# Optimization experiments

Hardware: AMD Instinct MI355X
Metric: run time of the kernel (lower is better)

The kernel has to match this reference:

```python
import jax, jax.numpy as jnp
import numpy as np

EPS = 1e-5  # torch LayerNorm default

def _ln(x, g, b):
    mu = jnp.mean(x, -1, keepdims=True)
    var = jnp.mean((x - mu) ** 2, -1, keepdims=True)
    return (x - mu) * jax.lax.rsqrt(var + EPS) * g + b

def _xavier(key, shape):
    fan_in, fan_out = shape[-2], shape[-1]
    s = (2.0 / (fan_in + fan_out)) ** 0.5
    return jax.random.normal(key, shape, dtype=jnp.float32) * s

def setup_inputs() -> dict:
    key = jax.random.key(0)
    ks = jax.random.split(key, 24)
    N, E, B = 10000, 160000, 64
    D, M, FF, K = 128, 32, 32, 5
    EIN = 2 * FF + 1 + 2 * D          # 321
    inp = {}
    inp["coords"] = jax.random.normal(ks[0], (N, 3), dtype=jnp.float32)
    inp["atomids"] = jax.random.randint(ks[1], (N,), 0, 11)
    inp["edge_index"] = jax.random.randint(ks[2], (2, E), 0, N)
    inp["batch"] = jnp.sort(jax.random.randint(ks[3], (N,), 0, B))
    inp["num_graphs"] = B
    inp["emb"] = _xavier(ks[4], (11, D))
    # stacked per-kernel EGNN params (leading dim K=5)
    inp["keW1"] = _xavier(ks[5], (K, EIN, 2 * EIN)); inp["keb1"] = jnp.zeros((K, 2 * EIN))
    inp["keW2"] = _xavier(ks[6], (K, 2 * EIN, M));   inp["keb2"] = jnp.zeros((K, M))
    inp["keng"] = jnp.ones((K, M));   inp["kenb"] = jnp.zeros((K, M))
    inp["kn1g"] = jnp.ones((K, D));   inp["kn1b"] = jnp.zeros((K, D))
    inp["knW1"] = _xavier(ks[7], (K, D + M, 2 * D)); inp["knb1"] = jnp.zeros((K, 2 * D))
    inp["knW2"] = _xavier(ks[8], (K, 2 * D, D));     inp["knb2"] = jnp.zeros((K, D))
    inp["kn2g"] = jnp.ones((K, D));   inp["kn2b"] = jnp.zeros((K, D))
    # fnn: (K+1)*D = 768 -> 256 -> 256 -> 256
    inp["fW0"] = _xavier(ks[9], ((K + 1) * D, 256)); inp["fb0"] = jnp.zeros((256,))
    inp["fW1"] = _xavier(ks[10], (256, 256));        inp["fb1"] = jnp.zeros((256,))
    inp["fW2"] = _xavier(ks[11], (256, 256));        inp["fb2"] = jnp.zeros((256,))
    # fnn2: 256 -> 256 -> 256 -> 1
    inp["gW0"] = _xavier(ks[12], (256, 256));        inp["gb0"] = jnp.zeros((256,))
    inp["gW1"] = _xavier(ks[13], (256, 256));        inp["gb1"] = jnp.zeros((256,))
    inp["gW2"] = _xavier(ks[14], (256, 1));          inp["gb2"] = jnp.zeros((1,))
    return inp

def reference(coords, atomids, edge_index, batch, num_graphs, emb,
              keW1, keb1, keW2, keb2, keng, kenb, kn1g, kn1b,
              knW1, knb1, knW2, knb2, kn2g, kn2b,
              fW0, fb0, fW1, fb1, fW2, fb2,
              gW0, gb0, gW1, gb1, gW2, gb2):
    silu = jax.nn.silu
    N = coords.shape[0]
    src, dst = edge_index[0], edge_index[1]  # x_j = x[src], x_i = x[dst]
    feats = emb[atomids]                                  # [N,128]
    # coords are never updated across kernels -> fourier edge attr computed once
    rel = coords[src] - coords[dst]                       # [E,3]
    d = jnp.sum(rel * rel, -1, keepdims=True)             # [E,1] squared distance
    scales = 2.0 ** jnp.arange(32, dtype=coords.dtype)
    xs = d / scales                                       # [E,32]
    ea = jnp.concatenate([jnp.sin(xs), jnp.cos(xs), d], -1)  # [E,65]
    ones_e = jnp.ones((src.shape[0], 1), feats.dtype)
    deg = jax.ops.segment_sum(ones_e, dst, num_segments=N)   # [N,1]
    deg = jnp.maximum(deg, 1.0)
    feat_list = [feats]
    for k in range(keW1.shape[0]):
        # edge message MLP
        m = jnp.concatenate([feats[dst], feats[src], ea], -1)        # [E,321]
        h = silu(m @ keW1[k] + keb1[k])                              # [E,642]
        m_ij = silu(h @ keW2[k] + keb2[k])                           # [E,32]
        m_ij = _ln(m_ij, keng[k], kenb[k])
        # scatter-mean aggregate to target nodes
        m_i = jax.ops.segment_sum(m_ij, dst, num_segments=N) / deg   # [N,32]
        m_i = _ln(m_i, keng[k], kenb[k])  # (original reuses edge_norm1)
        # node update MLP with residual
        hf = _ln(feats, kn1g[k], kn1b[k])
        h2 = silu(jnp.concatenate([hf, m_i], -1) @ knW1[k] + knb1[k])
        h2 = h2 @ knW2[k] + knb2[k]
        h2 = _ln(h2, kn2g[k], kn2b[k])
        feats = feats + h2
        feat_list.append(feats)
    f = silu(jnp.concatenate(feat_list, -1))              # [N,768]
    f = silu(f @ fW0 + fb0)
    f = silu(f @ fW1 + fb1)
    f = silu(f @ fW2 + fb2)
    gs = jax.ops.segment_sum(f, batch, num_segments=num_graphs)
    gc = jax.ops.segment_sum(jnp.ones((N, 1), f.dtype), batch, num_segments=num_graphs)
    g = gs / jnp.maximum(gc, 1.0)                         # [B,256] scatter_mean
    g = silu(g @ gW0 + gb0)
    g = silu(g @ gW1 + gb1)
    return g @ gW2 + gb2                                  # [B,1]
```

## Files before the change

kernel.cpp:

```cpp
#include <hip/hip_runtime.h>
#include <cstdint>
#include <cstddef>


#define DEV __device__ __forceinline__

typedef __attribute__((ext_vector_type(8))) short bf16x8;
typedef __attribute__((ext_vector_type(4))) float f32x4;

DEV float siluf(float x) { return x / (1.f + __expf(-x)); }

DEV unsigned short f2bf(float f) {
  unsigned u = __float_as_uint(f);
  unsigned r = u + 0x7FFFu + ((u >> 16) & 1u);
  return (unsigned short)(r >> 16);
}
DEV float bf2f(unsigned short h) { return __uint_as_float(((unsigned)h) << 16); }

DEV f32x4 mfma16(bf16x8 a, bf16x8 b, f32x4 c) {
  return __builtin_amdgcn_mfma_f32_16x16x32_bf16(a, b, c, 0, 0, 0);
}

DEV void unpack8(bf16x8 v, float* o) {
#pragma unroll
  for (int j = 0; j < 8; ++j) o[j] = bf2f((unsigned short)v[j]);
}

__global__ __launch_bounds__(256) void k_gather(const int* __restrict__ atomids,
                                                const float* __restrict__ emb,
                                                float* __restrict__ feats_all,
                                                unsigned short* __restrict__ fH, int N) {
  int idx = blockIdx.x * 256 + threadIdx.x;
  if (idx >= N * 128) return;
  int i = idx >> 7, j = idx & 127;
  float v = emb[atomids[i] * 128 + j];
  size_t o = (size_t)i * 768 + j;
  feats_all[o] = v;
  fH[o] = f2bf(v);
}

__global__ __launch_bounds__(256) void k_edge_prep(const float* __restrict__ coords,
                                                   const int* __restrict__ ei, int E,
                                                   float* __restrict__ d_arr,
                                                   int* __restrict__ cnt) {
  int e = blockIdx.x * 256 + threadIdx.x;
  if (e >= E) return;
  int s = ei[e], t = ei[E + e];
  float dx = coords[3 * s + 0] - coords[3 * t + 0];
  float dy = coords[3 * s + 1] - coords[3 * t + 1];
  float dz = coords[3 * s + 2] - coords[3 * t + 2];
  d_arr[e] = dx * dx + dy * dy + dz * dz;
  atomicAdd(&cnt[t], 1);
}

__global__ __launch_bounds__(1024) void k_scan2(const int* __restrict__ cnt, int N,
                                                int* __restrict__ cursor,
                                                float* __restrict__ degf) {
  __shared__ int wsum[16];
  int tid = threadIdx.x;
  int chunk = (N + 1023) >> 10;
  int lo = tid * chunk, hi = min(N, lo + chunk);
  int s = 0;
  for (int i = lo; i < hi; ++i) s += cnt[i];
  int lane = tid & 63, wv = tid >> 6;
  int v = s;
#pragma unroll
  for (int off = 1; off < 64; off <<= 1) {
    int u = __shfl_up(v, off, 64);
    if (lane >= off) v += u;
  }
  if (lane == 63) wsum[wv] = v;
  __syncthreads();
  if (wv == 0 && lane < 16) {
    int w = wsum[lane];
#pragma unroll
    for (int off = 1; off < 16; off <<= 1) {
      int u = __shfl_up(w, off, 16);
      if (lane >= off) w += u;
    }
    wsum[lane] = w;
  }
  __syncthreads();
  int run = (wv ? wsum[wv - 1] : 0) + v - s;
  for (int i = lo; i < hi; ++i) {
    int c = cnt[i];
    cursor[i] = run;
    degf[i] = fmaxf((float)c, 1.f);
    run += c;
  }
}

__global__ __launch_bounds__(256) void k_scatter(const int* __restrict__ ei, int E,
                                                 const float* __restrict__ d_arr,
                                                 int* __restrict__ cursor,
                                                 int* __restrict__ ssrc,
                                                 int* __restrict__ sdst,
                                                 float* __restrict__ sd) {
  int e = blockIdx.x * 256 + threadIdx.x;
  if (e >= E) return;
  int s = ei[e], t = ei[E + e];
  int p = atomicAdd(&cursor[t], 1);
  ssrc[p] = s;
  sdst[p] = t;
  sd[p] = d_arr[e];
}

struct PPJob {
  const float* W;
  unsigned short* hi;
  unsigned short* lo;
  unsigned long long wStride, oStride;
  int ldw, K, Kpad, Nc, Npad, layers;
};
struct PPJobs { PPJob j[11]; };

__global__ __launch_bounds__(256) void k_prepack_all(PPJobs jobs) {
  PPJob jb = jobs.j[blockIdx.y];
  long long per = (long long)jb.Npad * jb.Kpad;
  long long idx = (long long)blockIdx.x * 256 + threadIdx.x;
  if (idx >= per * jb.layers) return;
  int layer = (int)(idx / per);
  int r = (int)(idx - (long long)layer * per);
  const float* W = jb.W + (size_t)layer * jb.wStride;
  int n = r / jb.Kpad, k = r - n * jb.Kpad;
  float v = (n < jb.Nc && k < jb.K) ? W[(size_t)k * jb.ldw + n] : 0.f;
  unsigned short h = f2bf(v);
  jb.hi[(size_t)layer * jb.oStride + r] = h;
  jb.lo[(size_t)layer * jb.oStride + r] = f2bf(v - bf2f(h));
}

__global__ __launch_bounds__(256) void gemm_bf(
    const unsigned short* __restrict__ AH, int lda,
    const unsigned short* __restrict__ BH, const unsigned short* __restrict__ BL, int ldb,
    const float* __restrict__ bias,
    float* __restrict__ C, int ldc,
    unsigned short* __restrict__ CH, int ldch,
    int M, int Ncols, int K, int actOut, int actA) {
  const int t = threadIdx.x;
  const int wave = t >> 6, lane = t & 63;
  const int nl = lane & 15, quad = lane >> 4;
  const int bm = blockIdx.x * 64 + wave * 16;
  const int bn = blockIdx.y * 64;
  f32x4 zero = {0.f, 0.f, 0.f, 0.f};
  f32x4 acc[4] = {zero, zero, zero, zero};
  for (int kb = 0; kb < K; kb += 32) {
    bf16x8 ah;
    int row = bm + nl;
    if (row < M) {
      ah = *(const bf16x8*)(AH + (size_t)row * lda + kb + quad * 8);
      if (actA) {
#pragma unroll
        for (int j = 0; j < 8; ++j)
          ah[j] = (short)f2bf(siluf(bf2f((unsigned short)ah[j])));
      }
    } else {
#pragma unroll
      for (int j = 0; j < 8; ++j) ah[j] = 0;
    }
#pragma unroll
    for (int tn = 0; tn < 4; ++tn) {
      size_t boff = (size_t)(bn + tn * 16 + nl) * ldb + kb + quad * 8;
      bf16x8 bh = *(const bf16x8*)(BH + boff);
      bf16x8 bl = *(const bf16x8*)(BL + boff);
      acc[tn] = mfma16(ah, bh, acc[tn]);
      acc[tn] = mfma16(ah, bl, acc[tn]);
    }
  }
#pragma unroll
  for (int tn = 0; tn < 4; ++tn) {
    int c = bn + tn * 16 + nl;
    float bv = (bias && c < Ncols) ? bias[c] : 0.f;
#pragma unroll
    for (int r = 0; r < 4; ++r) {
      int rr = bm + quad * 4 + r;
      if (rr >= M) continue;
      float v = acc[tn][r] + bv;
      if (actOut) v = siluf(v);
      if (C && c < Ncols) C[(size_t)rr * ldc + c] = v;
      if (CH && c < Ncols) CH[(size_t)rr * ldch + c] = f2bf(v);
    }
  }
}

__global__ __launch_bounds__(256) void gemm_proj(
    const unsigned short* __restrict__ AH, int lda,
    const unsigned short* __restrict__ B1H, const unsigned short* __restrict__ B1L,
    const unsigned short* __restrict__ B2H, const unsigned short* __restrict__ B2L,
    const float* __restrict__ bias1,
    unsigned short* __restrict__ C1, unsigned short* __restrict__ C2,
    int planeN, int M) {
  const int y = blockIdx.y;
  const unsigned short* BH;
  const unsigned short* BL;
  const float* bias;
  unsigned short* CP;
  int yp;
  if (y < 11) { BH = B1H; BL = B1L; bias = bias1; CP = C1; yp = y; }
  else        { BH = B2H; BL = B2L; bias = nullptr; CP = C2; yp = y - 11; }
  const int t = threadIdx.x;
  const int wave = t >> 6, lane = t & 63;
  const int nl = lane & 15, quad = lane >> 4;
  const int bm = blockIdx.x * 128 + wave * 32;
  const int bn = yp * 64;
  f32x4 zero = {0.f, 0.f, 0.f, 0.f};
  f32x4 acc[2][4] = {{zero, zero, zero, zero}, {zero, zero, zero, zero}};
  for (int kb = 0; kb < 128; kb += 32) {
    bf16x8 ah[2];
#pragma unroll
    for (int h = 0; h < 2; ++h) {
      int row = bm + h * 16 + nl;
      if (row < M)
        ah[h] = *(const bf16x8*)(AH + (size_t)row * lda + kb + quad * 8);
      else
#pragma unroll
        for (int j = 0; j < 8; ++j) ah[h][j] = 0;
    }
#pragma unroll
    for (int tn = 0; tn < 4; ++tn) {
      size_t boff = (size_t)(bn + tn * 16 + nl) * 128 + kb + quad * 8;
      bf16x8 bh = *(const bf16x8*)(BH + boff);
      bf16x8 bl = *(const bf16x8*)(BL + boff);
#pragma unroll
      for (int h = 0; h < 2; ++h) {
        acc[h][tn] = mfma16(ah[h], bh, acc[h][tn]);
        acc[h][tn] = mfma16(ah[h], bl, acc[h][tn]);
      }
    }
  }
#pragma unroll
  for (int h = 0; h < 2; ++h) {
#pragma unroll
    for (int tn = 0; tn < 4; ++tn) {
      int c = bn + tn * 16 + nl;
      float bv = (bias && c < 642) ? bias[c] : 0.f;
#pragma unroll
      for (int r = 0; r < 4; ++r) {
        int rr = bm + h * 16 + quad * 4 + r;
        if (rr >= M) continue;
        CP[(size_t)yp * planeN + (size_t)rr * 64 + tn * 16 + nl] =
            f2bf(acc[h][tn][r] + bv);
      }
    }
  }
}

__global__ __launch_bounds__(256, 3) void k_edge_mfma(
    const unsigned short* __restrict__ Ap, const unsigned short* __restrict__ Bp,
    int planeN,
    const int* __restrict__ ssrc, const int* __restrict__ sdst,
    const float* __restrict__ sd_g, int E,
    const unsigned short* __restrict__ WeaT,
    const float* __restrict__ Wea64,
    const unsigned short* __restrict__ W2T,
    const float* __restrict__ b2v,
    const float* __restrict__ eng, const float* __restrict__ enb,
    float* __restrict__ msum) {
  __shared__ float sAB[4][16 * 68];
  __shared__ unsigned short sHh[4][16 * 72];
  __shared__ float sDs[64];
  __shared__ int sSrcS[64], sDstS[64];

  const int t = threadIdx.x;
  const int wave = t >> 6, lane = t & 63;
  const int nl = lane & 15, quad = lane >> 4;
  const int e0 = blockIdx.x * 64;

  if (lane < 16) {
    int el = wave * 16 + lane;
    int e = e0 + el;
    int ec = (e < E) ? e : (E - 1);
    sSrcS[el] = ssrc[ec];
    sDstS[el] = sdst[ec];
    sDs[el] = sd_g[ec];
  }
  const int r = lane >> 2, cq = lane & 3;
  const int elr = wave * 16 + r;
  const size_t aOff = (size_t)sDstS[elr] * 64 + cq * 16;
  const size_t bOff = (size_t)sSrcS[elr] * 64 + cq * 16;
  const float dR = sDs[elr];
  float* myAB = sAB[wave];
  unsigned short* myH = sHh[wave];

  bf16x8 pa0, pa1, pb0, pb1;
  bf16x8 w1[4][2], w2a[2][2], w2b[2][2];

  auto loadW1 = [&](int c) {
#pragma unroll
    for (int tn = 0; tn < 4; ++tn)
#pragma unroll
      for (int ks = 0; ks < 2; ++ks)
        w1[tn][ks] = *(const bf16x8*)(WeaT + (size_t)(c * 64 + tn * 16 + nl) * 64 +
                                      ks * 32 + quad * 8);
  };
  auto loadW2 = [&](int c, bf16x8(*w)[2]) {
#pragma unroll
    for (int tn = 0; tn < 2; ++tn)
#pragma unroll
      for (int ks = 0; ks < 2; ++ks)
        w[tn][ks] = *(const bf16x8*)(W2T + (size_t)(tn * 16 + nl) * 704 + c * 64 +
                                     ks * 32 + quad * 8);
  };
  auto issue = [&](int c) {
    const unsigned short* a = Ap + (size_t)c * planeN + aOff;
    const unsigned short* b = Bp + (size_t)c * planeN + bOff;
    pa0 = *(const bf16x8*)a;
    pa1 = *(const bf16x8*)(a + 8);
    pb0 = *(const bf16x8*)b;
    pb1 = *(const bf16x8*)(b + 8);
  };
  auto commit = [&](int c) {
    float za[16], zb[16], w[16];
    unpack8(pa0, za); unpack8(pa1, za + 8);
    unpack8(pb0, zb); unpack8(pb1, zb + 8);
    const int cb = c * 64 + cq * 16;
    if (cb + 15 < 642) {
#pragma unroll
      for (int j = 0; j < 4; ++j) {
        f32x4 wv = *(const f32x4*)(Wea64 + cb + 4 * j);
        w[4 * j] = wv.x; w[4 * j + 1] = wv.y; w[4 * j + 2] = wv.z; w[4 * j + 3] = wv.w;
      }
    } else {
#pragma unroll
      for (int u = 0; u < 16; ++u) w[u] = (cb + u < 642) ? Wea64[cb + u] : 0.f;
    }
#pragma unroll
    for (int j = 0; j < 4; ++j) {
      f32x4 o;
#pragma unroll
      for (int u = 0; u < 4; ++u) o[u] = za[4 * j + u] + zb[4 * j + u] + dR * w[4 * j + u];
      *(f32x4*)(myAB + r * 68 + cq * 16 + 4 * j) = o;
    }
  };

  issue(0);
  bf16x8 eaHi[2];
  {
    float d = sDs[wave * 16 + nl];
#pragma unroll
    for (int ks = 0; ks < 2; ++ks)
#pragma unroll
      for (int j = 0; j < 8; ++j) {
        int k = ks * 32 + quad * 8 + j;
        float arg = d * exp2f(-(float)(k & 31));
        float v = (k < 32) ? __sinf(arg) : __cosf(arg);
        eaHi[ks][j] = (short)f2bf(v);
      }
  }
  loadW1(0);
  loadW2(0, w2a);

  f32x4 zero = {0.f, 0.f, 0.f, 0.f};
  f32x4 macc[2] = {zero, zero};

#pragma unroll
  for (int c = 0; c < 11; ++c) {
    commit(c);
    if (c < 10) issue(c + 1);
    f32x4 acc1[4] = {zero, zero, zero, zero};
#pragma unroll
    for (int tn = 0; tn < 4; ++tn)
#pragma unroll
      for (int ks = 0; ks < 2; ++ks) acc1[tn] = mfma16(eaHi[ks], w1[tn][ks], acc1[tn]);
#pragma unroll
    for (int tn = 0; tn < 4; ++tn)
#pragma unroll
      for (int rr = 0; rr < 4; ++rr) {
        int lrow = quad * 4 + rr;
        float z = acc1[tn][rr] + myAB[lrow * 68 + tn * 16 + nl];
        myH[lrow * 72 + tn * 16 + nl] = f2bf(siluf(z));
      }
    if (c < 10) {
      loadW1(c + 1);
      loadW2(c + 1, (c & 1) ? w2a : w2b);
    }
    bf16x8(*w2)[2] = (c & 1) ? w2b : w2a;
#pragma unroll
    for (int ks = 0; ks < 2; ++ks) {
      bf16x8 ah = *(const bf16x8*)(myH + nl * 72 + ks * 32 + quad * 8);
#pragma unroll
      for (int tn = 0; tn < 2; ++tn) macc[tn] = mfma16(ah, w2[tn][ks], macc[tn]);
    }
  }

  float g0 = eng[nl], g1v = eng[16 + nl], bb0 = enb[nl], bb1 = enb[16 + nl];
  float bi0 = b2v[nl], bi1 = b2v[16 + nl];
  float* sMw = myAB;
#pragma unroll
  for (int rr = 0; rr < 4; ++rr) {
    float v0 = siluf(macc[0][rr] + bi0);
    float v1 = siluf(macc[1][rr] + bi1);
    float s = v0 + v1;
    float ss = v0 * v0 + v1 * v1;
#pragma unroll
    for (int m = 1; m < 16; m <<= 1) {
      s += __shfl_xor(s, m, 16);
      ss += __shfl_xor(ss, m, 16);
    }
    float mu = s * (1.f / 32.f);
    float var = ss * (1.f / 32.f) - mu * mu;
    float rs = rsqrtf(var + 1e-5f);
    int lr = quad * 4 + rr;
    sMw[lr * 33 + nl] = (v0 - mu) * rs * g0 + bb0;
    sMw[lr * 33 + 16 + nl] = (v1 - mu) * rs * g1v + bb1;
  }
  __syncthreads();
  {
    int col = t & 31, seg = t >> 5;
    float acc = 0.f;
    int cur = -1;
#pragma unroll
    for (int i = 0; i < 8; ++i) {
      int e = seg * 8 + i;
      int dn = (e0 + e < E) ? sDstS[e] : -1;
      if (dn != cur) {
        if (cur >= 0) atomicAdd(&msum[(size_t)cur * 32 + col], acc);
        acc = 0.f;
        cur = dn;
      }
      if (dn >= 0) acc += sAB[e >> 4][(e & 15) * 33 + col];
    }
    if (cur >= 0) atomicAdd(&msum[(size_t)cur * 32 + col], acc);
  }
}

__global__ __launch_bounds__(256) void k_node_ln(
    const float* __restrict__ msum, const float* __restrict__ deg,
    const float* __restrict__ featsAll, int k,
    const float* __restrict__ n1g, const float* __restrict__ n1b,
    const float* __restrict__ eng, const float* __restrict__ enb,
    unsigned short* __restrict__ hcatH, int N) {
  int node = blockIdx.x * 4 + (threadIdx.x >> 6);
  int lane = threadIdx.x & 63;
  if (node >= N) return;
  const float* fr = featsAll + (size_t)node * 768 + k * 128;
  float x0 = fr[lane], x1 = fr[64 + lane];
  float s = x0 + x1;
#pragma unroll
  for (int m = 1; m < 64; m <<= 1) s += __shfl_xor(s, m, 64);
  float mu = s * (1.f / 128.f);
  float d0 = x0 - mu, d1 = x1 - mu;
  float v = d0 * d0 + d1 * d1;
#pragma unroll
  for (int m = 1; m < 64; m <<= 1) v += __shfl_xor(v, m, 64);
  float rstd = rsqrtf(v * (1.f / 128.f) + 1e-5f);
  size_t hb = (size_t)node * 160;
  hcatH[hb + lane] = f2bf(d0 * rstd * n1g[lane] + n1b[lane]);
  hcatH[hb + 64 + lane] = f2bf(d1 * rstd * n1g[64 + lane] + n1b[64 + lane]);
  float dg = deg[node];
  int col = lane & 31;
  float y = msum[(size_t)node * 32 + col] / dg;
  float sy = y;
#pragma unroll
  for (int m = 1; m < 32; m <<= 1) sy += __shfl_xor(sy, m, 32);
  float mu2 = sy * (1.f / 32.f);
  float dy = y - mu2;
  float vy = dy * dy;
#pragma unroll
  for (int m = 1; m < 32; m <<= 1) vy += __shfl_xor(vy, m, 32);
  float rstd2 = rsqrtf(vy * (1.f / 32.f) + 1e-5f);
  if (lane < 32) hcatH[hb + 128 + col] = f2bf(dy * rstd2 * eng[col] + enb[col]);
}

__global__ __launch_bounds__(256) void k_n2_resid(
    const unsigned short* __restrict__ t1H,
    const unsigned short* __restrict__ BH, const unsigned short* __restrict__ BL,
    const float* __restrict__ b2,
    const float* __restrict__ n2g, const float* __restrict__ n2b,
    float* __restrict__ featsAll, unsigned short* __restrict__ fH, int k, int N) {
  const int t = threadIdx.x;
  const int wave = t >> 6, lane = t & 63;
  const int nl = lane & 15, quad = lane >> 4;
  const int bm = blockIdx.x * 64 + wave * 16;
  f32x4 zero = {0.f, 0.f, 0.f, 0.f};
  f32x4 acc[8] = {zero, zero, zero, zero, zero, zero, zero, zero};
  for (int kb = 0; kb < 256; kb += 32) {
    bf16x8 ah;
    int row = bm + nl;
    if (row < N)
      ah = *(const bf16x8*)(t1H + (size_t)row * 256 + kb + quad * 8);
    else
#pragma unroll
      for (int j = 0; j < 8; ++j) ah[j] = 0;
#pragma unroll
    for (int tn = 0; tn < 8; ++tn) {
      size_t boff = (size_t)(tn * 16 + nl) * 256 + kb + quad * 8;
      bf16x8 bh = *(const bf16x8*)(BH + boff);
      bf16x8 bl = *(const bf16x8*)(BL + boff);
      acc[tn] = mfma16(ah, bh, acc[tn]);
      acc[tn] = mfma16(ah, bl, acc[tn]);
    }
  }
  float bv[8], gv[8], bb[8];
#pragma unroll
  for (int tn = 0; tn < 8; ++tn) {
    int col = tn * 16 + nl;
    bv[tn] = b2[col];
    gv[tn] = n2g[col];
    bb[tn] = n2b[col];
  }
#pragma unroll
  for (int r = 0; r < 4; ++r) {
    int row = bm + quad * 4 + r;
    float v[8];
    float s = 0.f, ss = 0.f;
#pragma unroll
    for (int tn = 0; tn < 8; ++tn) {
      v[tn] = acc[tn][r] + bv[tn];
      s += v[tn];
      ss += v[tn] * v[tn];
    }
#pragma unroll
    for (int m = 1; m < 16; m <<= 1) {
      s += __shfl_xor(s, m, 16);
      ss += __shfl_xor(ss, m, 16);
    }
    float mu = s * (1.f / 128.f);
    float var = ss * (1.f / 128.f) - mu * mu;
    float rs = rsqrtf(var + 1e-5f);
    if (row < N) {
      const float* fk = featsAll + (size_t)row * 768 + k * 128;
      size_t ob = (size_t)row * 768 + (k + 1) * 128;
#pragma unroll
      for (int tn = 0; tn < 8; ++tn) {
        int col = tn * 16 + nl;
        float o = fk[col] + (v[tn] - mu) * rs * gv[tn] + bb[tn];
        featsAll[ob + col] = o;
        fH[ob + col] = f2bf(o);
      }
    }
  }
}

__global__ __launch_bounds__(256) void k_pool2(const float* __restrict__ f,
                                               const int* __restrict__ batch,
                                               float* __restrict__ gsum,
                                               float* __restrict__ gcnt, int N) {
  int n0 = blockIdx.x * 64;
  int col = threadIdx.x;
  float acc = 0.f;
  int cur = -1;
  for (int i = 0; i < 64; ++i) {
    int n = n0 + i;
    if (n >= N) break;
    int b = batch[n];
    if (b != cur) {
      if (cur >= 0) atomicAdd(&gsum[cur * 256 + col], acc);
      acc = 0.f;
      cur = b;
    }
    acc += f[(size_t)n * 256 + col];
  }
  if (cur >= 0) atomicAdd(&gsum[cur * 256 + col], acc);
  if (threadIdx.x == 0) {
    int cnt = 0;
    cur = -1;
    for (int i = 0; i < 64; ++i) {
      int n = n0 + i;
      if (n >= N) break;
      int b = batch[n];
      if (b != cur) {
        if (cur >= 0) atomicAdd(&gcnt[cur], (float)cnt);
        cnt = 0;
        cur = b;
      }
      cnt++;
    }
    if (cur >= 0) atomicAdd(&gcnt[cur], (float)cnt);
  }
}

__global__ void k_gdiv(float* gsum, const float* gcnt, unsigned short* gH) {
  int b = blockIdx.x, j = threadIdx.x;
  float v = gsum[b * 256 + j] / fmaxf(gcnt[b], 1.f);
  gH[b * 256 + j] = f2bf(v);
}

__global__ void k_gout(const float* __restrict__ g2, const float* __restrict__ gW2,
                       const float* __restrict__ gb2, float* __restrict__ out) {
  int b = threadIdx.x;
  if (b >= 64) return;
  float s = gb2[0];
  for (int j = 0; j < 256; ++j) s += g2[b * 256 + j] * gW2[j];
  out[b] = s;
}

extern "C" void kernel_launch(void* const* d_in, const int* in_sizes, int n_in,
                              void* d_out, int out_size, void* d_ws, size_t ws_size,
                              hipStream_t stream) {
  const float* coords = (const float*)d_in[0];
  const int* atomids = (const int*)d_in[1];
  const int* ei = (const int*)d_in[2];
  const int* batch = (const int*)d_in[3];
  const float* emb = (const float*)d_in[5];
  const float* keW1 = (const float*)d_in[6];
  const float* keb1 = (const float*)d_in[7];
  const float* keW2 = (const float*)d_in[8];
  const float* keb2 = (const float*)d_in[9];
  const float* keng = (const float*)d_in[10];
  const float* kenb = (const float*)d_in[11];
  const float* kn1g = (const float*)d_in[12];
  const float* kn1b = (const float*)d_in[13];
  const float* knW1 = (const float*)d_in[14];
  const float* knb1 = (const float*)d_in[15];
  const float* knW2 = (const float*)d_in[16];
  const float* knb2 = (const float*)d_in[17];
  const float* kn2g = (const float*)d_in[18];
  const float* kn2b = (const float*)d_in[19];
  const float* fW0 = (const float*)d_in[20];
  const float* fb0 = (const float*)d_in[21];
  const float* fW1 = (const float*)d_in[22];
  const float* fb1 = (const float*)d_in[23];
  const float* fW2 = (const float*)d_in[24];
  const float* fb2 = (const float*)d_in[25];
  const float* gW0 = (const float*)d_in[26];
  const float* gb0 = (const float*)d_in[27];
  const float* gW1 = (const float*)d_in[28];
  const float* gb1 = (const float*)d_in[29];
  const float* gW2 = (const float*)d_in[30];
  const float* gb2 = (const float*)d_in[31];

  const int N = in_sizes[0] / 3;
  const int E = in_sizes[2] / 2;
  const int planeN = N * 64;

  size_t off = 0;
  auto alloc = [&](size_t n) {
    float* p = (float*)d_ws + off;
    off += (n + 63) & ~(size_t)63;
    return p;
  };
  float* feats_all = alloc((size_t)N * 768);
  float* d_arr = alloc(E);
  float* degf = alloc(N);
  float* msum = alloc((size_t)N * 32);
  float* f1 = alloc((size_t)N * 256);
  float* gsum = alloc(64 * 256);
  float* gcnt = alloc(64);
  float* g2 = alloc(64 * 256);
  int* cnt = (int*)alloc(N);
  int* cursor = (int*)alloc(N);
  int* ssrc = (int*)alloc(E);
  int* sdst = (int*)alloc(E);
  float* sd = alloc(E);

  unsigned short* ubase = (unsigned short*)(alloc(0));
  size_t uoff = 0;
  auto ualloc = [&](size_t n) {
    unsigned short* p = ubase + uoff;
    uoff += (n + 63) & ~(size_t)63;
    return p;
  };
  unsigned short* fH = ualloc((size_t)N * 768);
  unsigned short* ApU = ualloc((size_t)11 * planeN);
  unsigned short* BpU = ualloc((size_t)11 * planeN);
  unsigned short* hcatH = ualloc((size_t)N * 160);
  unsigned short* t1H = ualloc((size_t)N * 256);
  unsigned short* fAH = ualloc((size_t)N * 256);
  unsigned short* fBH = ualloc((size_t)N * 256);
  unsigned short* gH = ualloc(64 * 256);
  unsigned short* g1H = ualloc(64 * 256);
  const size_t sDst_ = 704 * 128, sSrc_ = 704 * 128, sEa_ = 704 * 64;
  const size_t sW2_ = 32 * 704, sN1_ = 256 * 160, sN2_ = 128 * 256;
  unsigned short* PdstH = ualloc(5 * sDst_); unsigned short* PdstL = ualloc(5 * sDst_);
  unsigned short* PsrcH = ualloc(5 * sSrc_); unsigned short* PsrcL = ualloc(5 * sSrc_);
  unsigned short* PeaH = ualloc(5 * sEa_);   unsigned short* PeaL = ualloc(5 * sEa_);
  unsigned short* PW2H = ualloc(5 * sW2_);   unsigned short* PW2L = ualloc(5 * sW2_);
  unsigned short* Pn1H = ualloc(5 * sN1_);   unsigned short* Pn1L = ualloc(5 * sN1_);
  unsigned short* Pn2H = ualloc(5 * sN2_);   unsigned short* Pn2L = ualloc(5 * sN2_);
  unsigned short* Pf0H = ualloc(256 * 768);  unsigned short* Pf0L = ualloc(256 * 768);
  unsigned short* Pf1H = ualloc(256 * 256);  unsigned short* Pf1L = ualloc(256 * 256);
  unsigned short* Pf2H = ualloc(256 * 256);  unsigned short* Pf2L = ualloc(256 * 256);
  unsigned short* Pg0H = ualloc(256 * 256);  unsigned short* Pg0L = ualloc(256 * 256);
  unsigned short* Pg1H = ualloc(256 * 256);  unsigned short* Pg1L = ualloc(256 * 256);

  PPJobs jobs;
  auto setJob = [&](int i, const float* W, size_t wStr, int ldw, int K, int Kpad,
                    int Nc, int Npad, unsigned short* hi, unsigned short* lo,
                    size_t oStr, int layers) {
    jobs.j[i] = PPJob{W, hi, lo, (unsigned long long)wStr, (unsigned long long)oStr,
                      ldw, K, Kpad, Nc, Npad, layers};
  };
  setJob(0, keW1, (size_t)321 * 642, 642, 128, 128, 642, 704, PdstH, PdstL, sDst_, 5);
  setJob(1, keW1 + 128 * 642, (size_t)321 * 642, 642, 128, 128, 642, 704, PsrcH, PsrcL, sSrc_, 5);
  setJob(2, keW1 + 256 * 642, (size_t)321 * 642, 642, 64, 64, 642, 704, PeaH, PeaL, sEa_, 5);
  setJob(3, keW2, (size_t)642 * 32, 32, 642, 704, 32, 32, PW2H, PW2L, sW2_, 5);
  setJob(4, knW1, (size_t)160 * 256, 256, 160, 160, 256, 256, Pn1H, Pn1L, sN1_, 5);
  setJob(5, knW2, (size_t)256 * 128, 128, 256, 256, 128, 128, Pn2H, Pn2L, sN2_, 5);
  setJob(6, fW0, 0, 256, 768, 768, 256, 256, Pf0H, Pf0L, 0, 1);
  setJob(7, fW1, 0, 256, 256, 256, 256, 256, Pf1H, Pf1L, 0, 1);
  setJob(8, fW2, 0, 256, 256, 256, 256, 256, Pf2H, Pf2L, 0, 1);
  setJob(9, gW0, 0, 256, 256, 256, 256, 256, Pg0H, Pg0L, 0, 1);
  setJob(10, gW1, 0, 256, 256, 256, 256, 256, Pg1H, Pg1L, 0, 1);
  k_prepack_all<<<dim3(1760, 11), 256, 0, stream>>>(jobs);

  k_gather<<<(N * 128 + 255) / 256, 256, 0, stream>>>(atomids, emb, feats_all, fH, N);
  hipMemsetAsync(cnt, 0, (size_t)N * sizeof(int), stream);
  k_edge_prep<<<(E + 255) / 256, 256, 0, stream>>>(coords, ei, E, d_arr, cnt);
  k_scan2<<<1, 1024, 0, stream>>>(cnt, N, cursor, degf);
  k_scatter<<<(E + 255) / 256, 256, 0, stream>>>(ei, E, d_arr, cursor, ssrc, sdst, sd);

  const int MT128 = (N + 127) / 128;
  const int MT64 = (N + 63) / 64;
  for (int k = 0; k < 5; ++k) {
    gemm_proj<<<dim3(MT128, 22), 256, 0, stream>>>(
        fH + k * 128, 768,
        PdstH + k * sDst_, PdstL + k * sDst_,
        PsrcH + k * sSrc_, PsrcL + k * sSrc_,
        keb1 + k * 642, ApU, BpU, planeN, N);
    hipMemsetAsync(msum, 0, (size_t)N * 32 * sizeof(float), stream);
    k_edge_mfma<<<(E + 63) / 64, 256, 0, stream>>>(
        ApU, BpU, planeN, ssrc, sdst, sd, E,
        PeaH + k * sEa_,
        keW1 + (size_t)k * 321 * 642 + (size_t)320 * 642,
        PW2H + k * sW2_,
        keb2 + k * 32, keng + k * 32, kenb + k * 32, msum);
    k_node_ln<<<(N + 3) / 4, 256, 0, stream>>>(
        msum, degf, feats_all, k, kn1g + k * 128, kn1b + k * 128,
        keng + k * 32, kenb + k * 32, hcatH, N);
    gemm_bf<<<dim3(MT64, 4), 256, 0, stream>>>(
        hcatH, 160, Pn1H + k * sN1_, Pn1L + k * sN1_, 160,
        knb1 + k * 256, nullptr, 0, t1H, 256, N, 256, 160, 1, 0);
    k_n2_resid<<<MT64, 256, 0, stream>>>(
        t1H, Pn2H + k * sN2_, Pn2L + k * sN2_, knb2 + k * 128,
        kn2g + k * 128, kn2b + k * 128, feats_all, fH, k, N);
  }

  gemm_bf<<<dim3(MT64, 4), 256, 0, stream>>>(
      fH, 768, Pf0H, Pf0L, 768, fb0, nullptr, 0, fAH, 256, N, 256, 768, 1, 1);
  gemm_bf<<<dim3(MT64, 4), 256, 0, stream>>>(
      fAH, 256, Pf1H, Pf1L, 256, fb1, nullptr, 0, fBH, 256, N, 256, 256, 1, 0);
  gemm_bf<<<dim3(MT64, 4), 256, 0, stream>>>(
      fBH, 256, Pf2H, Pf2L, 256, fb2, f1, 256, nullptr, 0, N, 256, 256, 1, 0);

  hipMemsetAsync(gsum, 0, 64 * 256 * sizeof(float), stream);
  hipMemsetAsync(gcnt, 0, 64 * sizeof(float), stream);
  k_pool2<<<(N + 63) / 64, 256, 0, stream>>>(f1, batch, gsum, gcnt, N);
  k_gdiv<<<64, 256, 0, stream>>>(gsum, gcnt, gH);
  gemm_bf<<<dim3(1, 4), 256, 0, stream>>>(
      gH, 256, Pg0H, Pg0L, 256, gb0, nullptr, 0, g1H, 256, 64, 256, 256, 1, 0);
  gemm_bf<<<dim3(1, 4), 256, 0, stream>>>(
      g1H, 256, Pg1H, Pg1L, 256, gb1, g2, 256, nullptr, 0, 64, 256, 256, 1, 0);
  k_gout<<<1, 64, 0, stream>>>(g2, gW2, gb2, (float*)d_out);
}
```

Measured before the change: 1.808 ms.

## Deepen edge-kernel prefetch to two stages and fuse dst/src projection tiles

The edge MFMA kernel now double-buffers both the gathered A/B projection rows and the W2 fragments, issuing loads two chunks ahead instead of one, so gather latency is hidden behind more compute. gemm_proj is restructured so each block handles 64 rows and computes both the dst and src projections for the same column slice, sharing one A-fragment load across eight accumulator tiles instead of splitting the work across separate grid-y blocks. The msum memset is moved before the projection GEMM. The cost is higher register pressure in both kernels, which may reduce occupancy.

```diff
diff --git a/kernel.cpp b/kernel.cpp
--- a/kernel.cpp
+++ b/kernel.cpp
@@ -189,57 +189,43 @@
     const float* __restrict__ bias1,
     unsigned short* __restrict__ C1, unsigned short* __restrict__ C2,
     int planeN, int M) {
-  const int y = blockIdx.y;
-  const unsigned short* BH;
-  const unsigned short* BL;
-  const float* bias;
-  unsigned short* CP;
-  int yp;
-  if (y < 11) { BH = B1H; BL = B1L; bias = bias1; CP = C1; yp = y; }
-  else        { BH = B2H; BL = B2L; bias = nullptr; CP = C2; yp = y - 11; }
+  const int yp = blockIdx.y;
   const int t = threadIdx.x;
   const int wave = t >> 6, lane = t & 63;
   const int nl = lane & 15, quad = lane >> 4;
-  const int bm = blockIdx.x * 128 + wave * 32;
-  const int bn = yp * 64;
+  const int bm = blockIdx.x * 64 + wave * 16;
   f32x4 zero = {0.f, 0.f, 0.f, 0.f};
-  f32x4 acc[2][4] = {{zero, zero, zero, zero}, {zero, zero, zero, zero}};
+  f32x4 acc[8] = {zero, zero, zero, zero, zero, zero, zero, zero};
   for (int kb = 0; kb < 128; kb += 32) {
-    bf16x8 ah[2];
-#pragma unroll
-    for (int h = 0; h < 2; ++h) {
-      int row = bm + h * 16 + nl;
-      if (row < M)
-        ah[h] = *(const bf16x8*)(AH + (size_t)row * lda + kb + quad * 8);
-      else
-#pragma unroll
-        for (int j = 0; j < 8; ++j) ah[h][j] = 0;
-    }
-#pragma unroll
-    for (int tn = 0; tn < 4; ++tn) {
-      size_t boff = (size_t)(bn + tn * 16 + nl) * 128 + kb + quad * 8;
+    bf16x8 ah;
+    int row = bm + nl;
+    if (row < M)
+      ah = *(const bf16x8*)(AH + (size_t)row * lda + kb + quad * 8);
+    else
+#pragma unroll
+      for (int j = 0; j < 8; ++j) ah[j] = 0;
+#pragma unroll
+    for (int tn = 0; tn < 8; ++tn) {
+      const unsigned short* BH = (tn < 4) ? B1H : B2H;
+      const unsigned short* BL = (tn < 4) ? B1L : B2L;
+      size_t boff = (size_t)(yp * 64 + (tn & 3) * 16 + nl) * 128 + kb + quad * 8;
       bf16x8 bh = *(const bf16x8*)(BH + boff);
       bf16x8 bl = *(const bf16x8*)(BL + boff);
-#pragma unroll
-      for (int h = 0; h < 2; ++h) {
-        acc[h][tn] = mfma16(ah[h], bh, acc[h][tn]);
-        acc[h][tn] = mfma16(ah[h], bl, acc[h][tn]);
-      }
-    }
-  }
-#pragma unroll
-  for (int h = 0; h < 2; ++h) {
-#pragma unroll
-    for (int tn = 0; tn < 4; ++tn) {
-      int c = bn + tn * 16 + nl;
-      float bv = (bias && c < 642) ? bias[c] : 0.f;
-#pragma unroll
-      for (int r = 0; r < 4; ++r) {
-        int rr = bm + h * 16 + quad * 4 + r;
-        if (rr >= M) continue;
-        CP[(size_t)yp * planeN + (size_t)rr * 64 + tn * 16 + nl] =
-            f2bf(acc[h][tn][r] + bv);
-      }
+      acc[tn] = mfma16(ah, bh, acc[tn]);
+      acc[tn] = mfma16(ah, bl, acc[tn]);
+    }
+  }
+#pragma unroll
+  for (int tn = 0; tn < 8; ++tn) {
+    int cc = yp * 64 + (tn & 3) * 16 + nl;
+    float bv = (tn < 4 && cc < 642) ? bias1[cc] : 0.f;
+    unsigned short* CP = (tn < 4) ? C1 : C2;
+#pragma unroll
+    for (int r = 0; r < 4; ++r) {
+      int rr = bm + quad * 4 + r;
+      if (rr >= M) continue;
+      CP[(size_t)yp * planeN + (size_t)rr * 64 + (tn & 3) * 16 + nl] =
+          f2bf(acc[tn][r] + bv);
     }
   }
 }
@@ -281,8 +267,8 @@
   float* myAB = sAB[wave];
   unsigned short* myH = sHh[wave];
 
-  bf16x8 pa0, pa1, pb0, pb1;
-  bf16x8 w1[4][2], w2a[2][2], w2b[2][2];
+  bf16x8 pa0[2], pa1[2], pb0[2], pb1[2];
+  bf16x8 w1[4][2], w2[2][2][2];
 
   auto loadW1 = [&](int c) {
 #pragma unroll
@@ -292,26 +278,26 @@
         w1[tn][ks] = *(const bf16x8*)(WeaT + (size_t)(c * 64 + tn * 16 + nl) * 64 +
                                       ks * 32 + quad * 8);
   };
-  auto loadW2 = [&](int c, bf16x8(*w)[2]) {
+  auto loadW2 = [&](int c, int buf) {
 #pragma unroll
     for (int tn = 0; tn < 2; ++tn)
 #pragma unroll
       for (int ks = 0; ks < 2; ++ks)
-        w[tn][ks] = *(const bf16x8*)(W2T + (size_t)(tn * 16 + nl) * 704 + c * 64 +
-                                     ks * 32 + quad * 8);
+        w2[buf][tn][ks] = *(const bf16x8*)(W2T + (size_t)(tn * 16 + nl) * 704 +
+                                           c * 64 + ks * 32 + quad * 8);
   };
-  auto issue = [&](int c) {
+  auto issue = [&](int c, int s) {
     const unsigned short* a = Ap + (size_t)c * planeN + aOff;
     const unsigned short* b = Bp + (size_t)c * planeN + bOff;
-    pa0 = *(const bf16x8*)a;
-    pa1 = *(const bf16x8*)(a + 8);
-    pb0 = *(const bf16x8*)b;
-    pb1 = *(const bf16x8*)(b + 8);
+    pa0[s] = *(const bf16x8*)a;
+    pa1[s] = *(const bf16x8*)(a + 8);
+    pb0[s] = *(const bf16x8*)b;
+    pb1[s] = *(const bf16x8*)(b + 8);
   };
-  auto commit = [&](int c) {
+  auto commit = [&](int c, int s) {
     float za[16], zb[16], w[16];
-    unpack8(pa0, za); unpack8(pa1, za + 8);
-    unpack8(pb0, zb); unpack8(pb1, zb + 8);
+    unpack8(pa0[s], za); unpack8(pa1[s], za + 8);
+    unpack8(pb0[s], zb); unpack8(pb1[s], zb + 8);
     const int cb = c * 64 + cq * 16;
     if (cb + 15 < 642) {
 #pragma unroll
@@ -332,7 +318,7 @@
     }
   };
 
-  issue(0);
+  issue(0, 0);
   bf16x8 eaHi[2];
   {
     float d = sDs[wave * 16 + nl];
@@ -347,15 +333,16 @@
       }
   }
   loadW1(0);
-  loadW2(0, w2a);
+  loadW2(0, 0);
+  loadW2(1, 1);
+  issue(1, 1);
 
   f32x4 zero = {0.f, 0.f, 0.f, 0.f};
   f32x4 macc[2] = {zero, zero};
 
 #pragma unroll
   for (int c = 0; c < 11; ++c) {
-    commit(c);
-    if (c < 10) issue(c + 1);
+    commit(c, c & 1);
     f32x4 acc1[4] = {zero, zero, zero, zero};
 #pragma unroll
     for (int tn = 0; tn < 4; ++tn)
@@ -369,16 +356,16 @@
         float z = acc1[tn][rr] + myAB[lrow * 68 + tn * 16 + nl];
         myH[lrow * 72 + tn * 16 + nl] = f2bf(siluf(z));
       }
-    if (c < 10) {
-      loadW1(c + 1);
-      loadW2(c + 1, (c & 1) ? w2a : w2b);
-    }
-    bf16x8(*w2)[2] = (c & 1) ? w2b : w2a;
+    if (c < 10) loadW1(c + 1);
 #pragma unroll
     for (int ks = 0; ks < 2; ++ks) {
       bf16x8 ah = *(const bf16x8*)(myH + nl * 72 + ks * 32 + quad * 8);
 #pragma unroll
-      for (int tn = 0; tn < 2; ++tn) macc[tn] = mfma16(ah, w2[tn][ks], macc[tn]);
+      for (int tn = 0; tn < 2; ++tn) macc[tn] = mfma16(ah, w2[c & 1][tn][ks], macc[tn]);
+    }
+    if (c < 9) {
+      loadW2(c + 2, c & 1);
+      issue(c + 2, c & 1);
     }
   }
 
@@ -699,15 +686,14 @@
   k_scan2<<<1, 1024, 0, stream>>>(cnt, N, cursor, degf);
   k_scatter<<<(E + 255) / 256, 256, 0, stream>>>(ei, E, d_arr, cursor, ssrc, sdst, sd);
 
-  const int MT128 = (N + 127) / 128;
   const int MT64 = (N + 63) / 64;
   for (int k = 0; k < 5; ++k) {
-    gemm_proj<<<dim3(MT128, 22), 256, 0, stream>>>(
+    hipMemsetAsync(msum, 0, (size_t)N * 32 * sizeof(float), stream);
+    gemm_proj<<<dim3(MT64, 11), 256, 0, stream>>>(
         fH + k * 128, 768,
         PdstH + k * sDst_, PdstL + k * sDst_,
         PsrcH + k * sSrc_, PsrcL + k * sSrc_,
         keb1 + k * 642, ApU, BpU, planeN, N);
-    hipMemsetAsync(msum, 0, (size_t)N * 32 * sizeof(float), stream);
     k_edge_mfma<<<(E + 63) / 64, 256, 0, stream>>>(
         ApU, BpU, planeN, ssrc, sdst, sd, E,
         PeaH + k * sEa_,
```

New measurement: 1.889 ms. +4.5%, slower.

## Deepen edge-kernel prefetch to two chunks ahead and raise occupancy hint

Applied to the files above, without the earlier changes.

The edge MFMA kernel now double-buffers its gathered A/B node-projection rows and its W2 fragments, issuing loads for chunk c+2 while chunk c is being computed instead of only c+1. The launch-bounds minimum-blocks hint also goes from 3 to 5. Both aim to hide global-load latency in this gather-heavy loop. The deeper prefetch needs more registers while the higher occupancy target caps registers per thread, so the compiler may spill.

```diff
diff --git a/kernel.cpp b/kernel.cpp
--- a/kernel.cpp
+++ b/kernel.cpp
@@ -244,7 +244,7 @@
   }
 }
 
-__global__ __launch_bounds__(256, 3) void k_edge_mfma(
+__global__ __launch_bounds__(256, 5) void k_edge_mfma(
     const unsigned short* __restrict__ Ap, const unsigned short* __restrict__ Bp,
     int planeN,
     const int* __restrict__ ssrc, const int* __restrict__ sdst,
@@ -281,8 +281,8 @@
   float* myAB = sAB[wave];
   unsigned short* myH = sHh[wave];
 
-  bf16x8 pa0, pa1, pb0, pb1;
-  bf16x8 w1[4][2], w2a[2][2], w2b[2][2];
+  bf16x8 pa0[2], pa1[2], pb0[2], pb1[2];
+  bf16x8 w1[4][2], w2[2][2][2];
 
   auto loadW1 = [&](int c) {
 #pragma unroll
@@ -292,26 +292,26 @@
         w1[tn][ks] = *(const bf16x8*)(WeaT + (size_t)(c * 64 + tn * 16 + nl) * 64 +
                                       ks * 32 + quad * 8);
   };
-  auto loadW2 = [&](int c, bf16x8(*w)[2]) {
+  auto loadW2 = [&](int c, int buf) {
 #pragma unroll
     for (int tn = 0; tn < 2; ++tn)
 #pragma unroll
       for (int ks = 0; ks < 2; ++ks)
-        w[tn][ks] = *(const bf16x8*)(W2T + (size_t)(tn * 16 + nl) * 704 + c * 64 +
-                                     ks * 32 + quad * 8);
+        w2[buf][tn][ks] = *(const bf16x8*)(W2T + (size_t)(tn * 16 + nl) * 704 +
+                                           c * 64 + ks * 32 + quad * 8);
   };
-  auto issue = [&](int c) {
+  auto issue = [&](int c, int s) {
     const unsigned short* a = Ap + (size_t)c * planeN + aOff;
     const unsigned short* b = Bp + (size_t)c * planeN + bOff;
-    pa0 = *(const bf16x8*)a;
-    pa1 = *(const bf16x8*)(a + 8);
-    pb0 = *(const bf16x8*)b;
-    pb1 = *(const bf16x8*)(b + 8);
+    pa0[s] = *(const bf16x8*)a;
+    pa1[s] = *(const bf16x8*)(a + 8);
+    pb0[s] = *(const bf16x8*)b;
+    pb1[s] = *(const bf16x8*)(b + 8);
   };
-  auto commit = [&](int c) {
+  auto commit = [&](int c, int s) {
     float za[16], zb[16], w[16];
-    unpack8(pa0, za); unpack8(pa1, za + 8);
-    unpack8(pb0, zb); unpack8(pb1, zb + 8);
+    unpack8(pa0[s], za); unpack8(pa1[s], za + 8);
+    unpack8(pb0[s], zb); unpack8(pb1[s], zb + 8);
     const int cb = c * 64 + cq * 16;
     if (cb + 15 < 642) {
 #pragma unroll
@@ -332,7 +332,7 @@
     }
   };
 
-  issue(0);
+  issue(0, 0);
   bf16x8 eaHi[2];
   {
     float d = sDs[wave * 16 + nl];
@@ -347,15 +347,16 @@
       }
   }
   loadW1(0);
-  loadW2(0, w2a);
+  loadW2(0, 0);
+  loadW2(1, 1);
+  issue(1, 1);
 
   f32x4 zero = {0.f, 0.f, 0.f, 0.f};
   f32x4 macc[2] = {zero, zero};
 
 #pragma unroll
   for (int c = 0; c < 11; ++c) {
-    commit(c);
-    if (c < 10) issue(c + 1);
+    commit(c, c & 1);
     f32x4 acc1[4] = {zero, zero, zero, zero};
 #pragma unroll
     for (int tn = 0; tn < 4; ++tn)
@@ -369,16 +370,16 @@
         float z = acc1[tn][rr] + myAB[lrow * 68 + tn * 16 + nl];
         myH[lrow * 72 + tn * 16 + nl] = f2bf(siluf(z));
       }
-    if (c < 10) {
-      loadW1(c + 1);
-      loadW2(c + 1, (c & 1) ? w2a : w2b);
-    }
-    bf16x8(*w2)[2] = (c & 1) ? w2b : w2a;
+    if (c < 10) loadW1(c + 1);
 #pragma unroll
     for (int ks = 0; ks < 2; ++ks) {
       bf16x8 ah = *(const bf16x8*)(myH + nl * 72 + ks * 32 + quad * 8);
 #pragma unroll
-      for (int tn = 0; tn < 2; ++tn) macc[tn] = mfma16(ah, w2[tn][ks], macc[tn]);
+      for (int tn = 0; tn < 2; ++tn) macc[tn] = mfma16(ah, w2[c & 1][tn][ks], macc[tn]);
+    }
+    if (c < 9) {
+      loadW2(c + 2, c & 1);
+      issue(c + 2, c & 1);
     }
   }
 
```

After: 1.820 ms. Within noise of the previous version (+0.6%).
